# Kernel optimization log

Hardware: AMD Instinct MI355X
Metric: run time of the kernel (lower is better)

Reference implementation:

```python
import jax, jax.numpy as jnp
import numpy as np


def setup_inputs() -> dict:
    key = jax.random.key(0)
    k1, k2 = jax.random.split(key)
    B, T, D = 32, 512, 512
    x = jax.random.normal(k1, (B, T, D), dtype=jnp.float32)
    duration = jax.random.randint(k2, (B, T), 0, 8, dtype=jnp.int32)
    return {"x": x, "duration": duration, "max_len": 2048}


def reference(x, duration, max_len):
    """Vectorized length regulator.

    x:        [B, T, D] float
    duration: [B, T] int frames per phoneme
    max_len:  static python int, padded output length

    Returns (output [B, max_len, D], mel_lengths [B]).
    Frame t of sample b copies phoneme j where j is the first index with
    cumsum(duration)[b, j] > t (i.e. searchsorted right). Frames beyond the
    total duration are zero-padded; sequences longer than max_len are truncated
    (mel_lengths reports the untruncated length, matching the torch module,
    with the all-zero-duration edge case yielding length 1).
    """
    B, T, D = x.shape
    csum = jnp.cumsum(duration, axis=1)            # [B, T]
    dur_sum = csum[:, -1]                          # [B]
    t = jnp.arange(max_len, dtype=csum.dtype)      # [max_len]
    # phoneme index for each output frame: searchsorted(csum[b], t, 'right')
    idx = jax.vmap(lambda c: jnp.searchsorted(c, t, side='right'))(csum)  # [B, max_len]
    idx = jnp.clip(idx, 0, T - 1)
    out = jnp.take_along_axis(x, idx[:, :, None], axis=1)  # [B, max_len, D]
    valid = t[None, :] < dur_sum[:, None]                  # [B, max_len]
    out = jnp.where(valid[:, :, None], out, jnp.zeros((), dtype=x.dtype))
    mel_lengths = jnp.maximum(dur_sum, 1).astype(jnp.int32)
    return out, mel_lengths
```

## Files before the change

### kernel.cpp

```cpp
#include <hip/hip_runtime.h>


#define BB      32
#define TT      512
#define DD      512
#define MAXLEN  2048

typedef float f4 __attribute__((ext_vector_type(4)));
typedef int   i4 __attribute__((ext_vector_type(4)));

__global__ __launch_bounds__(512) void lr_scan_kernel(
    const int* __restrict__ dur, int* __restrict__ idxt,
    float* __restrict__ mel_out) {
  __shared__ int wsum[8];
  const int b    = blockIdx.x;
  const int tid  = threadIdx.x;
  const int lane = tid & 63;
  const int wid  = tid >> 6;

  const int d = dur[b * TT + tid];
  int v = d;
#pragma unroll
  for (int off = 1; off < 64; off <<= 1) {
    int n = __shfl_up(v, off, 64);
    if (lane >= off) v += n;
  }
  if (lane == 63) wsum[wid] = v;
  __syncthreads();

  int woff = 0, dsum = 0;
#pragma unroll
  for (int i = 0; i < 8; ++i) {
    int w = wsum[i];
    dsum += w;
    if (i < wid) woff += w;
  }
  v += woff;

  if (tid == 0) mel_out[b] = (float)(dsum > 1 ? dsum : 1);

  int start = v - d;
  int end   = v;
  if (start > MAXLEN) start = MAXLEN;
  if (end   > MAXLEN) end   = MAXLEN;
  int* row = idxt + b * MAXLEN;
  for (int t = start; t < end; ++t) row[t] = tid;
  for (int t = dsum + tid; t < MAXLEN; t += TT) row[t] = -1;
}

__global__ __launch_bounds__(256) void lr_copy_kernel(
    const int* __restrict__ idxt, const f4* __restrict__ x,
    f4* __restrict__ out) {
  const int lane    = threadIdx.x & 63;
  const int gwave   = blockIdx.x * (256 / 64) + (threadIdx.x >> 6);
  const int nwaves  = gridDim.x * (256 / 64);
  const int ngroups = (BB * MAXLEN) / 4;
  const f4 zero = {0.f, 0.f, 0.f, 0.f};

  for (int grp = gwave; grp < ngroups; grp += nwaves) {
    const int b  = grp >> 9;
    const int t0 = (grp & 511) * 4;
    const i4 idx4 = *(const i4*)&idxt[b * MAXLEN + t0];
    const f4* xb = x + (size_t)b * (TT * (DD / 4));
    f4* ob = out + ((size_t)b * MAXLEN + t0) * (DD / 4) + lane;
#pragma unroll
    for (int f = 0; f < 4; ++f) {
      const int idx = idx4[f];
      f4 v0 = zero, v1 = zero;
      if (idx >= 0) {
        const f4* xr = xb + (size_t)idx * (DD / 4) + lane;
        v0 = xr[0];
        v1 = xr[64];
      }
      __builtin_nontemporal_store(v0, ob + f * (DD / 4));
      __builtin_nontemporal_store(v1, ob + f * (DD / 4) + 64);
    }
  }
}

extern "C" void kernel_launch(void* const* d_in, const int* in_sizes, int n_in,
                              void* d_out, int out_size, void* d_ws, size_t ws_size,
                              hipStream_t stream) {
  const float* x   = (const float*)d_in[0];
  const int*   dur = (const int*)d_in[1];
  float* out = (float*)d_out;
  float* mel_out = out + (size_t)BB * MAXLEN * DD;
  int* idxt = (int*)d_ws;

  lr_scan_kernel<<<BB, 512, 0, stream>>>(dur, idxt, mel_out);
  lr_copy_kernel<<<2048, 256, 0, stream>>>(idxt, (const f4*)x, (f4*)out);
}
```

Before: 173.5 us.

## Fuse scan and copy into single scatter kernel reading each phoneme once

```diff
diff --git a/kernel.cpp b/kernel.cpp
--- a/kernel.cpp
+++ b/kernel.cpp
@@ -5,21 +5,24 @@
 #define TT      512
 #define DD      512
 #define MAXLEN  2048
+#define RPF     (DD / 4)
 
 typedef float f4 __attribute__((ext_vector_type(4)));
-typedef int   i4 __attribute__((ext_vector_type(4)));
 
-__global__ __launch_bounds__(512) void lr_scan_kernel(
-    const int* __restrict__ dur, int* __restrict__ idxt,
-    float* __restrict__ mel_out) {
+__global__ __launch_bounds__(512) void lr_scatter_kernel(
+    const int* __restrict__ dur, const f4* __restrict__ x,
+    f4* __restrict__ out, float* __restrict__ mel_out) {
+  __shared__ int s[TT];
   __shared__ int wsum[8];
-  const int b    = blockIdx.x;
+
+  const int bid  = blockIdx.x;
+  const int b    = bid >> 5;
+  const int sub  = bid & 31;
   const int tid  = threadIdx.x;
   const int lane = tid & 63;
   const int wid  = tid >> 6;
 
-  const int d = dur[b * TT + tid];
-  int v = d;
+  int v = dur[b * TT + tid];
 #pragma unroll
   for (int off = 1; off < 64; off <<= 1) {
     int n = __shfl_up(v, off, 64);
@@ -27,7 +30,6 @@
   }
   if (lane == 63) wsum[wid] = v;
   __syncthreads();
-
   int woff = 0, dsum = 0;
 #pragma unroll
   for (int i = 0; i < 8; ++i) {
@@ -36,45 +38,41 @@
     if (i < wid) woff += w;
   }
   v += woff;
+  s[tid] = v;
+  __syncthreads();
 
-  if (tid == 0) mel_out[b] = (float)(dsum > 1 ? dsum : 1);
+  if (sub == 0 && tid == 0) {
+    mel_out[b] = (float)(dsum > 1 ? dsum : 1);
+  }
 
-  int start = v - d;
-  int end   = v;
-  if (start > MAXLEN) start = MAXLEN;
-  if (end   > MAXLEN) end   = MAXLEN;
-  int* row = idxt + b * MAXLEN;
-  for (int t = start; t < end; ++t) row[t] = tid;
-  for (int t = dsum + tid; t < MAXLEN; t += TT) row[t] = -1;
-}
+  const f4* xb = x + (size_t)b * TT * RPF;
+  f4* ob       = out + (size_t)b * MAXLEN * RPF;
 
-__global__ __launch_bounds__(256) void lr_copy_kernel(
-    const int* __restrict__ idxt, const f4* __restrict__ x,
-    f4* __restrict__ out) {
-  const int lane    = threadIdx.x & 63;
-  const int gwave   = blockIdx.x * (256 / 64) + (threadIdx.x >> 6);
-  const int nwaves  = gridDim.x * (256 / 64);
-  const int ngroups = (BB * MAXLEN) / 4;
+#pragma unroll
+  for (int jj = 0; jj < 2; ++jj) {
+    const int j = (sub << 4) + (wid << 1) + jj;
+    int start = (j > 0) ? s[j - 1] : 0;
+    int end   = s[j];
+    if (start > MAXLEN) start = MAXLEN;
+    if (end   > MAXLEN) end   = MAXLEN;
+    if (end > start) {
+      const f4* xr = xb + (size_t)j * RPF + lane;
+      const f4 v0 = xr[0];
+      const f4 v1 = xr[64];
+      f4* o = ob + (size_t)start * RPF + lane;
+      for (int t = start; t < end; ++t, o += RPF) {
+        o[0]  = v0;
+        o[64] = v1;
+      }
+    }
+  }
+
   const f4 zero = {0.f, 0.f, 0.f, 0.f};
-
-  for (int grp = gwave; grp < ngroups; grp += nwaves) {
-    const int b  = grp >> 9;
-    const int t0 = (grp & 511) * 4;
-    const i4 idx4 = *(const i4*)&idxt[b * MAXLEN + t0];
-    const f4* xb = x + (size_t)b * (TT * (DD / 4));
-    f4* ob = out + ((size_t)b * MAXLEN + t0) * (DD / 4) + lane;
-#pragma unroll
-    for (int f = 0; f < 4; ++f) {
-      const int idx = idx4[f];
-      f4 v0 = zero, v1 = zero;
-      if (idx >= 0) {
-        const f4* xr = xb + (size_t)idx * (DD / 4) + lane;
-        v0 = xr[0];
-        v1 = xr[64];
-      }
-      __builtin_nontemporal_store(v0, ob + f * (DD / 4));
-      __builtin_nontemporal_store(v1, ob + f * (DD / 4) + 64);
-    }
+  const int slot = (sub << 3) + wid;
+  for (int t = dsum + slot; t < MAXLEN; t += 256) {
+    f4* o = ob + (size_t)t * RPF + lane;
+    o[0]  = zero;
+    o[64] = zero;
   }
 }
 
@@ -85,8 +83,7 @@
   const int*   dur = (const int*)d_in[1];
   float* out = (float*)d_out;
   float* mel_out = out + (size_t)BB * MAXLEN * DD;
-  int* idxt = (int*)d_ws;
 
-  lr_scan_kernel<<<BB, 512, 0, stream>>>(dur, idxt, mel_out);
-  lr_copy_kernel<<<2048, 256, 0, stream>>>(idxt, (const f4*)x, (f4*)out);
+  lr_scatter_kernel<<<BB * 32, 512, 0, stream>>>(
+      dur, (const f4*)x, (f4*)out, mel_out);
 }
```

Measured after the change: 164.0 us. 1.06x faster.

## Replace persistent wave-per-frame copy loop with flat grid sweeping batch pairs

Applied to the files above, without the earlier changes.

```diff
diff --git a/kernel.cpp b/kernel.cpp
--- a/kernel.cpp
+++ b/kernel.cpp
@@ -5,9 +5,11 @@
 #define TT      512
 #define DD      512
 #define MAXLEN  2048
+#define RPF     (DD / 4)
+#define GTH     (1 << 19)
+#define NSWEEP  16
 
 typedef float f4 __attribute__((ext_vector_type(4)));
-typedef int   i4 __attribute__((ext_vector_type(4)));
 
 __global__ __launch_bounds__(512) void lr_scan_kernel(
     const int* __restrict__ dur, int* __restrict__ idxt,
@@ -48,32 +50,33 @@
   for (int t = dsum + tid; t < MAXLEN; t += TT) row[t] = -1;
 }
 
-__global__ __launch_bounds__(256) void lr_copy_kernel(
+__global__ __launch_bounds__(256) void lr_sweep_kernel(
     const int* __restrict__ idxt, const f4* __restrict__ x,
     f4* __restrict__ out) {
-  const int lane    = threadIdx.x & 63;
-  const int gwave   = blockIdx.x * (256 / 64) + (threadIdx.x >> 6);
-  const int nwaves  = gridDim.x * (256 / 64);
-  const int ngroups = (BB * MAXLEN) / 4;
+  const int g  = blockIdx.x * 256 + threadIdx.x;
+  const int d4 = g & (RPF - 1);
+  const int t  = (g >> 7) & (MAXLEN - 1);
+  const int hi = g >> 18;
   const f4 zero = {0.f, 0.f, 0.f, 0.f};
 
-  for (int grp = gwave; grp < ngroups; grp += nwaves) {
-    const int b  = grp >> 9;
-    const int t0 = (grp & 511) * 4;
-    const i4 idx4 = *(const i4*)&idxt[b * MAXLEN + t0];
-    const f4* xb = x + (size_t)b * (TT * (DD / 4));
-    f4* ob = out + ((size_t)b * MAXLEN + t0) * (DD / 4) + lane;
 #pragma unroll
-    for (int f = 0; f < 4; ++f) {
-      const int idx = idx4[f];
-      f4 v0 = zero, v1 = zero;
+  for (int h = 0; h < 2; ++h) {
+    int idxv[8];
+#pragma unroll
+    for (int k = 0; k < 8; ++k) {
+      const int b = 2 * (h * 8 + k) + hi;
+      idxv[k] = idxt[b * MAXLEN + t];
+    }
+#pragma unroll
+    for (int k = 0; k < 8; ++k) {
+      const int kk = h * 8 + k;
+      const int b  = 2 * kk + hi;
+      const int idx = idxv[k];
+      f4 v = zero;
       if (idx >= 0) {
-        const f4* xr = xb + (size_t)idx * (DD / 4) + lane;
-        v0 = xr[0];
-        v1 = xr[64];
+        v = x[((size_t)b * TT + idx) * RPF + d4];
       }
-      __builtin_nontemporal_store(v0, ob + f * (DD / 4));
-      __builtin_nontemporal_store(v1, ob + f * (DD / 4) + 64);
+      out[(size_t)g + (size_t)kk * GTH] = v;
     }
   }
 }
@@ -88,5 +91,5 @@
   int* idxt = (int*)d_ws;
 
   lr_scan_kernel<<<BB, 512, 0, stream>>>(dur, idxt, mel_out);
-  lr_copy_kernel<<<2048, 256, 0, stream>>>(idxt, (const f4*)x, (f4*)out);
+  lr_sweep_kernel<<<GTH / 256, 256, 0, stream>>>(idxt, (const f4*)x, (f4*)out);
 }
```

Result: faster. 168.8 us (-2.7%).
